# Kernel tuning notes

Measured on AMD Instinct MI355X. Metric: run time of the kernel, lower is better.

The kernel has to match this reference:

```python
import jax, jax.numpy as jnp
import numpy as np

# model dims
C_CH = 64      # channels C
M_DIM = 128    # state dim m
R = 8          # low-rank r
DG = 64        # token_dim d_g
CHUNK = 512    # chunk_len
B, H, W = 4, 256, 256


def setup_inputs() -> dict:
    key = jax.random.key(0)
    ks = jax.random.split(key, 12)
    n = jax.random.normal
    return {
        "x": n(ks[0], (B, C_CH, H, W), jnp.float32),
        "g": n(ks[1], (B, DG), jnp.float32),
        # 1x1 conv weights flattened to matrices
        "in_proj_w": n(ks[2], (M_DIM, C_CH), jnp.float32) * 0.05,
        "in_proj_b": jnp.zeros((M_DIM,), jnp.float32),
        "out_proj_w": n(ks[3], (C_CH, M_DIM), jnp.float32) * 0.05,  # Cbase; conv bias unused in forward
        "U_base": n(ks[4], (M_DIM, R), jnp.float32) * 0.02,
        "V_base": n(ks[5], (M_DIM, R), jnp.float32) * 0.02,
        "a_base": jnp.zeros((M_DIM,), jnp.float32),
        "mod_uv_w": n(ks[6], (2 * R, DG), jnp.float32) * 0.05,
        "mod_uv_b": jnp.zeros((2 * R,), jnp.float32),
        "mod_a_w": n(ks[7], (M_DIM, DG), jnp.float32) * 0.05,
        "mod_a_b": jnp.zeros((M_DIM,), jnp.float32),
        "mod_B_w": n(ks[8], (M_DIM, DG), jnp.float32) * 0.05,
        "mod_B_b": jnp.zeros((M_DIM,), jnp.float32),
        "mod_C_w": n(ks[9], (C_CH, DG), jnp.float32) * 0.05,
        "mod_C_b": jnp.zeros((C_CH,), jnp.float32),
        "h0": jnp.zeros((M_DIM,), jnp.float32),
    }


def reference(x, g, in_proj_w, in_proj_b, out_proj_w, U_base, V_base, a_base,
              mod_uv_w, mod_uv_b, mod_a_w, mod_a_b, mod_B_w, mod_B_b,
              mod_C_w, mod_C_b, h0):
    Bsz, Cch, Hh, Ww = x.shape
    # 1x1 conv in_proj
    x_proj = jnp.einsum('bchw,mc->bmhw', x, in_proj_w) + in_proj_b[None, :, None, None]
    # g-conditioned modulations
    uv = g @ mod_uv_w.T + mod_uv_b
    gU = jnp.clip(uv[:, :R], -0.5, 0.5)[:, None, :]          # (B,1,r)
    gV = jnp.clip(uv[:, R:], -0.5, 0.5)[:, None, :]          # (B,1,r)
    ga = jnp.clip(g @ mod_a_w.T + mod_a_b, -2.0, 2.0)        # (B,m)
    gB = jnp.clip(g @ mod_B_w.T + mod_B_b, -1.0, 1.0)        # (B,m)
    gC = jnp.clip(g @ mod_C_w.T + mod_C_b, -0.5, 0.5)        # (B,C)
    Ug = U_base[None] * (1.0 + gU)                            # (B,m,r)
    Vg = V_base[None] * (1.0 + gV)                            # (B,m,r)
    a = a_base[None] + ga                                     # (B,m)
    Cg = out_proj_w[None] * (1.0 + gC)[:, :, None]            # (B,C,m)

    L = Hh * Ww
    x_seq = x_proj.reshape(Bsz, M_DIM, L).transpose(0, 2, 1)  # (B,L,m)
    x_seq = x_seq * (1.0 + gB)[:, None, :]
    pad = (-L) % CHUNK
    if pad > 0:
        x_seq = jnp.pad(x_seq, ((0, 0), (0, pad), (0, 0)))
    Lp = L + pad
    Mch = Lp // CHUNK
    # (T, B, K, m): scan over time within chunks, chunks run in parallel
    x_chunks = x_seq.reshape(Bsz, Mch, CHUNK, M_DIM).transpose(2, 0, 1, 3)
    h_init = jnp.broadcast_to(h0, (Bsz, Mch, M_DIM))

    def step(h, xt):
        v = jnp.einsum('bmr,bkm->bkr', Vg, h)                 # V^T h
        Av = jnp.einsum('bmr,bkr->bkm', Ug, v)                # U (V^T h)
        h_new = jnp.clip(Av + h * a[:, None, :] + xt, -10.0, 10.0)
        yc = jnp.clip(jnp.einsum('bcm,bkm->bkc', Cg, h_new), -10.0, 10.0)
        return h_new, yc

    _, ys = jax.lax.scan(step, h_init, x_chunks)              # (T,B,K,C)
    out_flat = ys.transpose(1, 2, 0, 3).reshape(Bsz, Lp, Cch)[:, :L, :]
    return out_flat.transpose(0, 2, 1).reshape(Bsz, Cch, Hh, Ww)
```

## Files before the change

### kernel.cpp

```cpp
#include <hip/hip_runtime.h>
#include <hip/hip_fp16.h>

#define L_TOT 65536

#define WS_UG   0
#define WS_VG   4096
#define WS_A    8192
#define WS_GB1  8704
#define WS_WHP  12288
#define WS_WLP  16384
#define WS_CGP  32768
#define WS_XS   65536

typedef __attribute__((ext_vector_type(8))) short short8;
typedef __attribute__((ext_vector_type(4))) float f32x4;
typedef _Float16 half8 __attribute__((ext_vector_type(8)));

__device__ __forceinline__ unsigned bf16rne(float f) {
    unsigned u = __builtin_bit_cast(unsigned, f);
    return (u + 0x7fffu + ((u >> 16) & 1u)) >> 16;
}
__device__ __forceinline__ float bfhi(unsigned u) {
    return __builtin_bit_cast(float, u << 16);
}
__device__ __forceinline__ unsigned f16pk(float a, float b) {
    __half2 h = __floats2half2_rn(a, b);
    return __builtin_bit_cast(unsigned, h);
}

__global__ __launch_bounds__(128) void mod_kernel(
    const float* __restrict__ g, const float* __restrict__ in_proj_w,
    const float* __restrict__ U_base, const float* __restrict__ V_base,
    const float* __restrict__ a_base, const float* __restrict__ out_proj_w,
    const float* __restrict__ mod_uv_w, const float* __restrict__ mod_uv_b,
    const float* __restrict__ mod_a_w, const float* __restrict__ mod_a_b,
    const float* __restrict__ mod_B_w, const float* __restrict__ mod_B_b,
    const float* __restrict__ mod_C_w, const float* __restrict__ mod_C_b,
    float* __restrict__ ws)
{
    __shared__ float gsh[64];
    __shared__ float uvs[16];
    __shared__ float gCs[64];
    const int b = blockIdx.x, tid = threadIdx.x;
    if (tid < 64) gsh[tid] = g[b * 64 + tid];
    __syncthreads();
    if (tid < 16) {
        float s = mod_uv_b[tid];
        for (int d = 0; d < 64; ++d) s += mod_uv_w[tid * 64 + d] * gsh[d];
        uvs[tid] = fminf(0.5f, fmaxf(-0.5f, s));
    }
    float ga_v, gB_v;
    {
        float s = mod_a_b[tid];
        for (int d = 0; d < 64; ++d) s += mod_a_w[tid * 64 + d] * gsh[d];
        ga_v = fminf(2.0f, fmaxf(-2.0f, s));
    }
    {
        float s = mod_B_b[tid];
        for (int d = 0; d < 64; ++d) s += mod_B_w[tid * 64 + d] * gsh[d];
        gB_v = 1.0f + fminf(1.0f, fmaxf(-1.0f, s));
    }
    if (tid < 64) {
        float s = mod_C_b[tid];
        for (int d = 0; d < 64; ++d) s += mod_C_w[tid * 64 + d] * gsh[d];
        gCs[tid] = 1.0f + fminf(0.5f, fmaxf(-0.5f, s));
    }
    __syncthreads();
    for (int idx = tid; idx < 1024; idx += 128) {
        int m = idx >> 3, r = idx & 7;
        ws[WS_UG + (b * 128 + m) * 8 + r] = U_base[m * 8 + r] * (1.0f + uvs[r]);
        ws[WS_VG + (b * 128 + m) * 8 + r] = V_base[m * 8 + r] * (1.0f + uvs[8 + r]);
    }
    ws[WS_A   + b * 128 + tid] = a_base[tid] + ga_v;
    ws[WS_GB1 + b * 128 + tid] = gB_v;
    unsigned* CgP = (unsigned*)(ws + WS_CGP);
    for (int idx = tid; idx < 4096; idx += 128) {
        int c = idx >> 6, j = idx & 63;
        float s = gCs[c];
        float c0 = out_proj_w[c * 128 + 2 * j]     * s;
        float c1 = out_proj_w[c * 128 + 2 * j + 1] * s;
        CgP[(b * 64 + c) * 64 + j] = f16pk(c0, c1);
    }
    if (b == 0) {
        unsigned* WhP = (unsigned*)(ws + WS_WHP);
        unsigned* WlP = (unsigned*)(ws + WS_WLP);
        for (int idx = tid; idx < 4096; idx += 128) {
            int m = idx >> 5, j = idx & 31;
            float w0 = in_proj_w[m * 64 + 2 * j];
            float w1 = in_proj_w[m * 64 + 2 * j + 1];
            unsigned u0 = bf16rne(w0), u1 = bf16rne(w1);
            WhP[idx] = u0 | (u1 << 16);
            float r0 = w0 - bfhi(u0);
            float r1 = w1 - bfhi(u1);
            WlP[idx] = bf16rne(r0) | (bf16rne(r1) << 16);
        }
    }
}

__global__ __launch_bounds__(256) void inproj_mfma(
    const float* __restrict__ x, const unsigned* __restrict__ WhP,
    const unsigned* __restrict__ WlP, const float* __restrict__ bias,
    const float* __restrict__ ws, unsigned* __restrict__ xs16)
{
    __shared__ __align__(16) unsigned XhS[64 * 36];
    __shared__ __align__(16) unsigned XlS[64 * 36];
    const int tid = threadIdx.x;
    const int b = blockIdx.y;
    const int l0 = blockIdx.x * 64;

    {
        const int l_st = tid & 63, cpg = tid >> 6;
        #pragma unroll
        for (int s = 0; s < 8; ++s) {
            int cp = cpg * 8 + s;
            float x0 = x[(size_t)(b * 64 + 2 * cp) * L_TOT + l0 + l_st];
            float x1 = x[(size_t)(b * 64 + 2 * cp + 1) * L_TOT + l0 + l_st];
            unsigned u0 = bf16rne(x0), u1 = bf16rne(x1);
            XhS[l_st * 36 + cp] = u0 | (u1 << 16);
            float r0 = x0 - bfhi(u0);
            float r1 = x1 - bfhi(u1);
            XlS[l_st * 36 + cp] = bf16rne(r0) | (bf16rne(r1) << 16);
        }
    }
    const int lane = tid & 63, wv = tid >> 6;
    const int row16 = lane & 15, grp = lane >> 4;

    short8 Ah[2][2], Al[2][2];
    #pragma unroll
    for (int t = 0; t < 2; ++t) {
        const int mrow = (2 * wv + t) * 16 + row16;
        #pragma unroll
        for (int kc = 0; kc < 2; ++kc) {
            Ah[t][kc] = __builtin_bit_cast(short8,
                *(const uint4*)(WhP + mrow * 32 + kc * 16 + grp * 4));
            Al[t][kc] = __builtin_bit_cast(short8,
                *(const uint4*)(WlP + mrow * 32 + kc * 16 + grp * 4));
        }
    }
    __syncthreads();

    #pragma unroll
    for (int ti = 0; ti < 4; ++ti) {
        const int lcol = ti * 16 + row16;
        short8 Bh[2], Bl[2];
        #pragma unroll
        for (int kc = 0; kc < 2; ++kc) {
            Bh[kc] = __builtin_bit_cast(short8,
                *(const uint4*)&XhS[lcol * 36 + kc * 16 + grp * 4]);
            Bl[kc] = __builtin_bit_cast(short8,
                *(const uint4*)&XlS[lcol * 36 + kc * 16 + grp * 4]);
        }
        #pragma unroll
        for (int t = 0; t < 2; ++t) {
            f32x4 acc = {0.f, 0.f, 0.f, 0.f};
            acc = __builtin_amdgcn_mfma_f32_16x16x32_bf16(Ah[t][0], Bh[0], acc, 0, 0, 0);
            acc = __builtin_amdgcn_mfma_f32_16x16x32_bf16(Ah[t][1], Bh[1], acc, 0, 0, 0);
            acc = __builtin_amdgcn_mfma_f32_16x16x32_bf16(Ah[t][0], Bl[0], acc, 0, 0, 0);
            acc = __builtin_amdgcn_mfma_f32_16x16x32_bf16(Ah[t][1], Bl[1], acc, 0, 0, 0);
            acc = __builtin_amdgcn_mfma_f32_16x16x32_bf16(Al[t][0], Bh[0], acc, 0, 0, 0);
            acc = __builtin_amdgcn_mfma_f32_16x16x32_bf16(Al[t][1], Bh[1], acc, 0, 0, 0);
            const int mb = (2 * wv + t) * 16 + 4 * grp;
            const int l = l0 + lcol;
            float4 bi = *(const float4*)(bias + mb);
            float4 gb = *(const float4*)(ws + WS_GB1 + b * 128 + mb);
            float v0 = (acc[0] + bi.x) * gb.x;
            float v1 = (acc[1] + bi.y) * gb.y;
            float v2 = (acc[2] + bi.z) * gb.z;
            float v3 = (acc[3] + bi.w) * gb.w;
            uint2 pk = {f16pk(v0, v1), f16pk(v2, v3)};
            *(uint2*)(xs16 + ((size_t)b * L_TOT + l) * 64 + (mb >> 1)) = pk;
        }
    }
}

__global__ __launch_bounds__(64, 1) void scan_kernel(
    const unsigned* __restrict__ xs16, const float* __restrict__ ws,
    const unsigned* __restrict__ CgP, const float* __restrict__ h0,
    float* __restrict__ out)
{
    __shared__ __align__(16) unsigned Hs[16 * 68];
    const int lane = threadIdx.x;
    const int bb = blockIdx.x >> 7, k = blockIdx.x & 127;
    const int m0 = 2 * lane;
    const int lp = lane & 7;
    const int row16 = lane & 15, grp = lane >> 4;

    float VgP0[8], VgP1[8], U0x[8], U1x[8];
    {
        const float* vg = ws + WS_VG + (bb * 128 + m0) * 8;
        const float* ug = ws + WS_UG + (bb * 128 + m0) * 8;
        #pragma unroll
        for (int j = 0; j < 8; ++j) {
            int r = j ^ lp;
            VgP0[j] = vg[r];     VgP1[j] = vg[8 + r];
            U0x[j]  = ug[r];     U1x[j]  = ug[8 + r];
        }
    }
    const float a0 = ws[WS_A + bb * 128 + m0];
    const float a1 = ws[WS_A + bb * 128 + m0 + 1];
    float ha = h0[m0], hb = h0[m0 + 1];

    half8 Af[4][4];
    #pragma unroll
    for (int ct = 0; ct < 4; ++ct)
        #pragma unroll
        for (int kc = 0; kc < 4; ++kc) {
            const unsigned* p = CgP + (bb * 64 + ct * 16 + row16) * 64 + kc * 16 + grp * 4;
            Af[ct][kc] = __builtin_bit_cast(half8, *(const uint4*)p);
        }

    const unsigned* xsp = xs16 + ((size_t)bb * L_TOT + (size_t)k * 512) * 64 + lane;
    float* ob[4];
    #pragma unroll
    for (int ct = 0; ct < 4; ++ct)
        ob[ct] = out + (size_t)(bb * 64 + ct * 16 + grp * 4) * L_TOT + k * 512 + row16;

    unsigned xqA[16], xqB[16];
    auto prefetch = [&](unsigned (&xq)[16], int seg) {
        const unsigned* xb = xsp + (size_t)seg * 1024;
        #pragma unroll
        for (int i = 0; i < 16; ++i) xq[i] = xb[(size_t)i * 64];
    };

    const float fz = 0.0f;

    auto do_seg = [&](const unsigned (&xq)[16], int t16) {
        #pragma unroll
        for (int i = 0; i < 16; ++i) {
            const float2 xv = __half22float2(__builtin_bit_cast(__half2, xq[i]));
            float p0 = fmaf(VgP1[0], hb, VgP0[0] * ha);
            float p1 = fmaf(VgP1[1], hb, VgP0[1] * ha);
            float p2 = fmaf(VgP1[2], hb, VgP0[2] * ha);
            float p3 = fmaf(VgP1[3], hb, VgP0[3] * ha);
            float p4 = fmaf(VgP1[4], hb, VgP0[4] * ha);
            float p5 = fmaf(VgP1[5], hb, VgP0[5] * ha);
            float p6 = fmaf(VgP1[6], hb, VgP0[6] * ha);
            float p7 = fmaf(VgP1[7], hb, VgP0[7] * ha);
            asm volatile(
                "s_nop 1\n\t"
                "v_add_f32_dpp %0, %1, %0 quad_perm:[1,0,3,2] row_mask:0xf bank_mask:0xf bound_ctrl:1\n\t"
                "v_add_f32_dpp %2, %3, %2 quad_perm:[1,0,3,2] row_mask:0xf bank_mask:0xf bound_ctrl:1\n\t"
                "v_add_f32_dpp %5, %4, %5 quad_perm:[1,0,3,2] row_mask:0xf bank_mask:0xf bound_ctrl:1\n\t"
                "v_add_f32_dpp %7, %6, %7 quad_perm:[1,0,3,2] row_mask:0xf bank_mask:0xf bound_ctrl:1\n\t"
                "s_nop 1\n\t"
                "v_add_f32_dpp %0, %2, %0 quad_perm:[2,3,0,1] row_mask:0xf bank_mask:0xf bound_ctrl:1\n\t"
                "v_add_f32_dpp %7, %5, %7 quad_perm:[2,3,0,1] row_mask:0xf bank_mask:0xf bound_ctrl:1\n\t"
                "s_nop 1\n\t"
                "v_add_f32_dpp %0, %7, %0 row_half_mirror row_mask:0xf bank_mask:0xf bound_ctrl:1\n\t"
                : "+v"(p0), "+v"(p1), "+v"(p2), "+v"(p3),
                  "+v"(p4), "+v"(p5), "+v"(p6), "+v"(p7));
            p0 += __builtin_bit_cast(float, __builtin_amdgcn_ds_swizzle(
                      __builtin_bit_cast(int, p0), 0x201F));
            p0 += __builtin_bit_cast(float, __builtin_amdgcn_ds_swizzle(
                      __builtin_bit_cast(int, p0), 0x401F));
            p0 += __shfl_xor(p0, 32);
            float vr1, vr2, vr3, vr4, vr5, vr6, vr7;
            asm volatile(
                "s_nop 1\n\t"
                "v_add_f32_dpp %0, %7, %8 quad_perm:[1,0,3,2] row_mask:0xf bank_mask:0xf bound_ctrl:1\n\t"
                "v_add_f32_dpp %1, %7, %8 quad_perm:[2,3,0,1] row_mask:0xf bank_mask:0xf bound_ctrl:1\n\t"
                "v_add_f32_dpp %2, %7, %8 quad_perm:[3,2,1,0] row_mask:0xf bank_mask:0xf bound_ctrl:1\n\t"
                "v_add_f32_dpp %6, %7, %8 row_half_mirror row_mask:0xf bank_mask:0xf bound_ctrl:1\n\t"
                "s_nop 1\n\t"
                "v_add_f32_dpp %5, %6, %8 quad_perm:[1,0,3,2] row_mask:0xf bank_mask:0xf bound_ctrl:1\n\t"
                "v_add_f32_dpp %4, %6, %8 quad_perm:[2,3,0,1] row_mask:0xf bank_mask:0xf bound_ctrl:1\n\t"
                "v_add_f32_dpp %3, %6, %8 quad_perm:[3,2,1,0] row_mask:0xf bank_mask:0xf bound_ctrl:1\n\t"
                : "=&v"(vr1), "=&v"(vr2), "=&v"(vr3), "=&v"(vr4),
                  "=&v"(vr5), "=&v"(vr6), "=&v"(vr7)
                : "v"(p0), "v"(fz));
            float c0 = fmaf(vr1, U0x[1], p0 * U0x[0]);
            c0 = fmaf(vr2, U0x[2], c0);
            c0 = fmaf(vr3, U0x[3], c0);
            float c1 = vr4 * U0x[4];
            c1 = fmaf(vr5, U0x[5], c1);
            c1 = fmaf(vr6, U0x[6], c1);
            c1 = fmaf(vr7, U0x[7], c1);
            float av0 = c0 + c1;
            float d0 = fmaf(vr1, U1x[1], p0 * U1x[0]);
            d0 = fmaf(vr2, U1x[2], d0);
            d0 = fmaf(vr3, U1x[3], d0);
            float d1 = vr4 * U1x[4];
            d1 = fmaf(vr5, U1x[5], d1);
            d1 = fmaf(vr6, U1x[6], d1);
            d1 = fmaf(vr7, U1x[7], d1);
            float av1 = d0 + d1;
            ha = fminf(10.0f, fmaxf(-10.0f, fmaf(a0, ha, av0) + xv.x));
            hb = fminf(10.0f, fmaxf(-10.0f, fmaf(a1, hb, av1) + xv.y));
            Hs[i * 68 + lane] = f16pk(ha, hb);
        }
        half8 Bf[4];
        #pragma unroll
        for (int kc = 0; kc < 4; ++kc)
            Bf[kc] = __builtin_bit_cast(half8,
                *(const uint4*)&Hs[row16 * 68 + kc * 16 + grp * 4]);
        #pragma unroll
        for (int ct = 0; ct < 4; ++ct) {
            f32x4 acc = {0.0f, 0.0f, 0.0f, 0.0f};
            #pragma unroll
            for (int kc = 0; kc < 4; ++kc)
                acc = __builtin_amdgcn_mfma_f32_16x16x32_f16(Af[ct][kc], Bf[kc], acc, 0, 0, 0);
            #pragma unroll
            for (int r = 0; r < 4; ++r) {
                float y = fminf(10.0f, fmaxf(-10.0f, acc[r]));
                ob[ct][(size_t)r * L_TOT + t16 * 16] = y;
            }
        }
    };

    prefetch(xqA, 0);
    #pragma unroll 1
    for (int t16 = 0; t16 < 32; t16 += 2) {
        prefetch(xqB, t16 + 1);
        do_seg(xqA, t16);
        prefetch(xqA, (t16 + 2) & 31);
        do_seg(xqB, t16 + 1);
    }
}

extern "C" void kernel_launch(void* const* d_in, const int* in_sizes, int n_in,
                              void* d_out, int out_size, void* d_ws, size_t ws_size,
                              hipStream_t stream) {
    const float* x          = (const float*)d_in[0];
    const float* g          = (const float*)d_in[1];
    const float* in_proj_w  = (const float*)d_in[2];
    const float* in_proj_b  = (const float*)d_in[3];
    const float* out_proj_w = (const float*)d_in[4];
    const float* U_base     = (const float*)d_in[5];
    const float* V_base     = (const float*)d_in[6];
    const float* a_base     = (const float*)d_in[7];
    const float* mod_uv_w   = (const float*)d_in[8];
    const float* mod_uv_b   = (const float*)d_in[9];
    const float* mod_a_w    = (const float*)d_in[10];
    const float* mod_a_b    = (const float*)d_in[11];
    const float* mod_B_w    = (const float*)d_in[12];
    const float* mod_B_b    = (const float*)d_in[13];
    const float* mod_C_w    = (const float*)d_in[14];
    const float* mod_C_b    = (const float*)d_in[15];
    const float* h0         = (const float*)d_in[16];
    float* out = (float*)d_out;
    float* ws  = (float*)d_ws;
    unsigned* xs16 = (unsigned*)(ws + WS_XS);

    hipLaunchKernelGGL(mod_kernel, dim3(4), dim3(128), 0, stream,
                       g, in_proj_w, U_base, V_base, a_base, out_proj_w,
                       mod_uv_w, mod_uv_b, mod_a_w, mod_a_b,
                       mod_B_w, mod_B_b, mod_C_w, mod_C_b, ws);
    hipLaunchKernelGGL(inproj_mfma, dim3(1024, 4), dim3(256), 0, stream,
                       x, (const unsigned*)(ws + WS_WHP), (const unsigned*)(ws + WS_WLP),
                       in_proj_b, ws, xs16);
    hipLaunchKernelGGL(scan_kernel, dim3(512), dim3(64), 0, stream,
                       xs16, ws, (const unsigned*)(ws + WS_CGP), h0, out);
}
```

Baseline: 186.2 us.

## Fuse input projection GEMM into scan kernel with software-pipelined segments

```diff
diff --git a/kernel.cpp b/kernel.cpp
--- a/kernel.cpp
+++ b/kernel.cpp
@@ -10,7 +10,6 @@
 #define WS_WHP  12288
 #define WS_WLP  16384
 #define WS_CGP  32768
-#define WS_XS   65536
 
 typedef __attribute__((ext_vector_type(8))) short short8;
 typedef __attribute__((ext_vector_type(4))) float f32x4;
@@ -97,87 +96,13 @@
     }
 }
 
-__global__ __launch_bounds__(256) void inproj_mfma(
-    const float* __restrict__ x, const unsigned* __restrict__ WhP,
-    const unsigned* __restrict__ WlP, const float* __restrict__ bias,
-    const float* __restrict__ ws, unsigned* __restrict__ xs16)
+__global__ __launch_bounds__(64, 1) void scan_kernel(
+    const float* __restrict__ x, const float* __restrict__ ws,
+    const unsigned* __restrict__ WhP, const unsigned* __restrict__ WlP,
+    const float* __restrict__ bias, const unsigned* __restrict__ CgP,
+    const float* __restrict__ h0, float* __restrict__ out)
 {
-    __shared__ __align__(16) unsigned XhS[64 * 36];
-    __shared__ __align__(16) unsigned XlS[64 * 36];
-    const int tid = threadIdx.x;
-    const int b = blockIdx.y;
-    const int l0 = blockIdx.x * 64;
-
-    {
-        const int l_st = tid & 63, cpg = tid >> 6;
-        #pragma unroll
-        for (int s = 0; s < 8; ++s) {
-            int cp = cpg * 8 + s;
-            float x0 = x[(size_t)(b * 64 + 2 * cp) * L_TOT + l0 + l_st];
-            float x1 = x[(size_t)(b * 64 + 2 * cp + 1) * L_TOT + l0 + l_st];
-            unsigned u0 = bf16rne(x0), u1 = bf16rne(x1);
-            XhS[l_st * 36 + cp] = u0 | (u1 << 16);
-            float r0 = x0 - bfhi(u0);
-            float r1 = x1 - bfhi(u1);
-            XlS[l_st * 36 + cp] = bf16rne(r0) | (bf16rne(r1) << 16);
-        }
-    }
-    const int lane = tid & 63, wv = tid >> 6;
-    const int row16 = lane & 15, grp = lane >> 4;
-
-    short8 Ah[2][2], Al[2][2];
-    #pragma unroll
-    for (int t = 0; t < 2; ++t) {
-        const int mrow = (2 * wv + t) * 16 + row16;
-        #pragma unroll
-        for (int kc = 0; kc < 2; ++kc) {
-            Ah[t][kc] = __builtin_bit_cast(short8,
-                *(const uint4*)(WhP + mrow * 32 + kc * 16 + grp * 4));
-            Al[t][kc] = __builtin_bit_cast(short8,
-                *(const uint4*)(WlP + mrow * 32 + kc * 16 + grp * 4));
-        }
-    }
-    __syncthreads();
-
-    #pragma unroll
-    for (int ti = 0; ti < 4; ++ti) {
-        const int lcol = ti * 16 + row16;
-        short8 Bh[2], Bl[2];
-        #pragma unroll
-        for (int kc = 0; kc < 2; ++kc) {
-            Bh[kc] = __builtin_bit_cast(short8,
-                *(const uint4*)&XhS[lcol * 36 + kc * 16 + grp * 4]);
-            Bl[kc] = __builtin_bit_cast(short8,
-                *(const uint4*)&XlS[lcol * 36 + kc * 16 + grp * 4]);
-        }
-        #pragma unroll
-        for (int t = 0; t < 2; ++t) {
-            f32x4 acc = {0.f, 0.f, 0.f, 0.f};
-            acc = __builtin_amdgcn_mfma_f32_16x16x32_bf16(Ah[t][0], Bh[0], acc, 0, 0, 0);
-            acc = __builtin_amdgcn_mfma_f32_16x16x32_bf16(Ah[t][1], Bh[1], acc, 0, 0, 0);
-            acc = __builtin_amdgcn_mfma_f32_16x16x32_bf16(Ah[t][0], Bl[0], acc, 0, 0, 0);
-            acc = __builtin_amdgcn_mfma_f32_16x16x32_bf16(Ah[t][1], Bl[1], acc, 0, 0, 0);
-            acc = __builtin_amdgcn_mfma_f32_16x16x32_bf16(Al[t][0], Bh[0], acc, 0, 0, 0);
-            acc = __builtin_amdgcn_mfma_f32_16x16x32_bf16(Al[t][1], Bh[1], acc, 0, 0, 0);
-            const int mb = (2 * wv + t) * 16 + 4 * grp;
-            const int l = l0 + lcol;
-            float4 bi = *(const float4*)(bias + mb);
-            float4 gb = *(const float4*)(ws + WS_GB1 + b * 128 + mb);
-            float v0 = (acc[0] + bi.x) * gb.x;
-            float v1 = (acc[1] + bi.y) * gb.y;
-            float v2 = (acc[2] + bi.z) * gb.z;
-            float v3 = (acc[3] + bi.w) * gb.w;
-            uint2 pk = {f16pk(v0, v1), f16pk(v2, v3)};
-            *(uint2*)(xs16 + ((size_t)b * L_TOT + l) * 64 + (mb >> 1)) = pk;
-        }
-    }
-}
-
-__global__ __launch_bounds__(64, 1) void scan_kernel(
-    const unsigned* __restrict__ xs16, const float* __restrict__ ws,
-    const unsigned* __restrict__ CgP, const float* __restrict__ h0,
-    float* __restrict__ out)
-{
+    __shared__ __align__(16) unsigned xp[2][16 * 68];
     __shared__ __align__(16) unsigned Hs[16 * 68];
     const int lane = threadIdx.x;
     const int bb = blockIdx.x >> 7, k = blockIdx.x & 127;
@@ -209,25 +134,81 @@
             Af[ct][kc] = __builtin_bit_cast(half8, *(const uint4*)p);
         }
 
-    const unsigned* xsp = xs16 + ((size_t)bb * L_TOT + (size_t)k * 512) * 64 + lane;
+    const float* xgb = x + (size_t)(bb * 64) * L_TOT + (size_t)k * 512 + row16;
     float* ob[4];
     #pragma unroll
     for (int ct = 0; ct < 4; ++ct)
         ob[ct] = out + (size_t)(bb * 64 + ct * 16 + grp * 4) * L_TOT + k * 512 + row16;
 
-    unsigned xqA[16], xqB[16];
-    auto prefetch = [&](unsigned (&xq)[16], int seg) {
-        const unsigned* xb = xsp + (size_t)seg * 1024;
-        #pragma unroll
-        for (int i = 0; i < 16; ++i) xq[i] = xb[(size_t)i * 64];
+    const float fz = 0.0f;
+    float xf[16];
+
+    auto gemm_load = [&](int s) {
+        const float* xs_ = xgb + s * 16;
+        #pragma unroll
+        for (int kc = 0; kc < 2; ++kc)
+            #pragma unroll
+            for (int q = 0; q < 4; ++q) {
+                int c = kc * 32 + grp * 8 + 2 * q;
+                xf[kc * 8 + 2 * q]     = xs_[(size_t)c * L_TOT];
+                xf[kc * 8 + 2 * q + 1] = xs_[(size_t)(c + 1) * L_TOT];
+            }
     };
 
-    const float fz = 0.0f;
-
-    auto do_seg = [&](const unsigned (&xq)[16], int t16) {
+    auto gemm_compute = [&](int s) {
+        unsigned* xpd = xp[s & 1];
+        short8 Bh[2], Bl[2];
+        #pragma unroll
+        for (int kc = 0; kc < 2; ++kc) {
+            unsigned uh[4], ul[4];
+            #pragma unroll
+            for (int q = 0; q < 4; ++q) {
+                float f0 = xf[kc * 8 + 2 * q], f1 = xf[kc * 8 + 2 * q + 1];
+                unsigned u0 = bf16rne(f0), u1 = bf16rne(f1);
+                uh[q] = u0 | (u1 << 16);
+                float r0 = f0 - bfhi(u0);
+                float r1 = f1 - bfhi(u1);
+                ul[q] = bf16rne(r0) | (bf16rne(r1) << 16);
+            }
+            uint4 th = {uh[0], uh[1], uh[2], uh[3]};
+            uint4 tl = {ul[0], ul[1], ul[2], ul[3]};
+            Bh[kc] = __builtin_bit_cast(short8, th);
+            Bl[kc] = __builtin_bit_cast(short8, tl);
+        }
+        #pragma unroll
+        for (int mt = 0; mt < 8; ++mt) {
+            const int mrow = mt * 16 + row16;
+            short8 Ah0 = __builtin_bit_cast(short8, *(const uint4*)(WhP + mrow * 32 + grp * 4));
+            short8 Ah1 = __builtin_bit_cast(short8, *(const uint4*)(WhP + mrow * 32 + 16 + grp * 4));
+            short8 Al0 = __builtin_bit_cast(short8, *(const uint4*)(WlP + mrow * 32 + grp * 4));
+            short8 Al1 = __builtin_bit_cast(short8, *(const uint4*)(WlP + mrow * 32 + 16 + grp * 4));
+            f32x4 acc = {0.f, 0.f, 0.f, 0.f};
+            acc = __builtin_amdgcn_mfma_f32_16x16x32_bf16(Ah0, Bh[0], acc, 0, 0, 0);
+            acc = __builtin_amdgcn_mfma_f32_16x16x32_bf16(Ah1, Bh[1], acc, 0, 0, 0);
+            acc = __builtin_amdgcn_mfma_f32_16x16x32_bf16(Ah0, Bl[0], acc, 0, 0, 0);
+            acc = __builtin_amdgcn_mfma_f32_16x16x32_bf16(Ah1, Bl[1], acc, 0, 0, 0);
+            acc = __builtin_amdgcn_mfma_f32_16x16x32_bf16(Al0, Bh[0], acc, 0, 0, 0);
+            acc = __builtin_amdgcn_mfma_f32_16x16x32_bf16(Al1, Bh[1], acc, 0, 0, 0);
+            const int mb = mt * 16 + 4 * grp;
+            float4 bi = *(const float4*)(bias + mb);
+            float4 gb = *(const float4*)(ws + WS_GB1 + bb * 128 + mb);
+            float v0 = (acc[0] + bi.x) * gb.x;
+            float v1 = (acc[1] + bi.y) * gb.y;
+            float v2 = (acc[2] + bi.z) * gb.z;
+            float v3 = (acc[3] + bi.w) * gb.w;
+            const int mp = mt * 8 + grp * 2;
+            xpd[row16 * 68 + mp]     = f16pk(v0, v1);
+            xpd[row16 * 68 + mp + 1] = f16pk(v2, v3);
+        }
+    };
+
+    auto scan_seg = [&](int s) {
+        const unsigned* xpk = xp[s & 1];
+        unsigned xcur = xpk[lane];
         #pragma unroll
         for (int i = 0; i < 16; ++i) {
-            const float2 xv = __half22float2(__builtin_bit_cast(__half2, xq[i]));
+            unsigned xnxt = (i < 15) ? xpk[(i + 1) * 68 + lane] : 0u;
+            const float2 xv = __half22float2(__builtin_bit_cast(__half2, xcur));
             float p0 = fmaf(VgP1[0], hb, VgP0[0] * ha);
             float p1 = fmaf(VgP1[1], hb, VgP0[1] * ha);
             float p2 = fmaf(VgP1[2], hb, VgP0[2] * ha);
@@ -287,7 +268,11 @@
             ha = fminf(10.0f, fmaxf(-10.0f, fmaf(a0, ha, av0) + xv.x));
             hb = fminf(10.0f, fmaxf(-10.0f, fmaf(a1, hb, av1) + xv.y));
             Hs[i * 68 + lane] = f16pk(ha, hb);
-        }
+            xcur = xnxt;
+        }
+    };
+
+    auto y_burst = [&](int s) {
         half8 Bf[4];
         #pragma unroll
         for (int kc = 0; kc < 4; ++kc)
@@ -302,18 +287,19 @@
             #pragma unroll
             for (int r = 0; r < 4; ++r) {
                 float y = fminf(10.0f, fmaxf(-10.0f, acc[r]));
-                ob[ct][(size_t)r * L_TOT + t16 * 16] = y;
+                ob[ct][(size_t)r * L_TOT + s * 16] = y;
             }
         }
     };
 
-    prefetch(xqA, 0);
+    gemm_load(0);
+    gemm_compute(0);
     #pragma unroll 1
-    for (int t16 = 0; t16 < 32; t16 += 2) {
-        prefetch(xqB, t16 + 1);
-        do_seg(xqA, t16);
-        prefetch(xqA, (t16 + 2) & 31);
-        do_seg(xqB, t16 + 1);
+    for (int s = 0; s < 32; ++s) {
+        if (s < 31) gemm_load(s + 1);
+        scan_seg(s);
+        if (s < 31) gemm_compute(s + 1);
+        y_burst(s);
     }
 }
 
@@ -339,15 +325,12 @@
     const float* h0         = (const float*)d_in[16];
     float* out = (float*)d_out;
     float* ws  = (float*)d_ws;
-    unsigned* xs16 = (unsigned*)(ws + WS_XS);
 
     hipLaunchKernelGGL(mod_kernel, dim3(4), dim3(128), 0, stream,
                        g, in_proj_w, U_base, V_base, a_base, out_proj_w,
                        mod_uv_w, mod_uv_b, mod_a_w, mod_a_b,
                        mod_B_w, mod_B_b, mod_C_w, mod_C_b, ws);
-    hipLaunchKernelGGL(inproj_mfma, dim3(1024, 4), dim3(256), 0, stream,
-                       x, (const unsigned*)(ws + WS_WHP), (const unsigned*)(ws + WS_WLP),
-                       in_proj_b, ws, xs16);
     hipLaunchKernelGGL(scan_kernel, dim3(512), dim3(64), 0, stream,
-                       xs16, ws, (const unsigned*)(ws + WS_CGP), h0, out);
-}
+                       x, ws, (const unsigned*)(ws + WS_WHP), (const unsigned*)(ws + WS_WLP),
+                       in_proj_b, (const unsigned*)(ws + WS_CGP), h0, out);
+}
```

Result: slower. 279.9 us (+50.3%).
